# Optimization experiments

Hardware: AMD Instinct MI355X
Metric: run time of the kernel (lower is better)

The kernel has to match this reference:

```python
import jax, jax.numpy as jnp
import numpy as np

B, N, H = 128, 65536, 30  # batch, candidates per sample, horizon-7 steps


def setup_inputs() -> dict:
    key = jax.random.key(0)
    ks = jax.random.split(key, 8)
    proposal_feat = jax.random.normal(ks[0], (B, 64), dtype=jnp.float32)
    target_candidate = jax.random.normal(ks[1], (B, N, 2), dtype=jnp.float32)
    candidate = jax.random.normal(ks[2], (B * N, 2), dtype=jnp.float32)
    # confidence (class-1 prob) in [0.5, 1.0) so the mask conf[0] >= 0.5 keeps ALL n columns
    conf = 0.5 + 0.5 * jax.random.uniform(ks[3], (B, N), dtype=jnp.float32)
    RCNN_cls_result = jnp.stack([1.0 - conf, conf], axis=-1)  # [B, N, 2]
    offset = 0.1 * jax.random.normal(ks[4], (B, N, 2), dtype=jnp.float32)
    yaw_pred = jax.random.normal(ks[5], (B, 1), dtype=jnp.float32)
    y = jax.random.normal(ks[6], (B * H * 2,), dtype=jnp.float32)      # flat dx,dy deltas
    y_yaw = jax.random.normal(ks[7], (B * H,), dtype=jnp.float32)
    horizon = jnp.full((B,), H + 7, dtype=jnp.int32)  # all equal -> static shapes
    return {
        'proposal_feat': proposal_feat,
        'target_candidate': target_candidate,
        'candidate': candidate,
        'RCNN_cls_result': RCNN_cls_result,
        'offset': offset,
        'yaw_pred': yaw_pred,
        'y': y,
        'y_yaw': y_yaw,
        'horizon': horizon,
    }


def reference(proposal_feat, target_candidate, candidate, RCNN_cls_result,
              offset, yaw_pred, y, y_yaw, horizon):
    batch, n, _ = target_candidate.shape
    candidate_pos = candidate.reshape(batch, n, 2)
    # confidence filter: inputs guarantee conf[0] >= 0.5 everywhere -> keep all n
    conf = RCNN_cls_result[..., 1]                       # [B, n]
    order = jnp.argsort(-conf, axis=1)                   # descending per sample
    pred_pt = jnp.take_along_axis(candidate_pos, order[:, :, None], axis=1)  # [B, n, 2]
    pred_off = jnp.take_along_axis(offset, order[:, :, None], axis=1)        # [B, n, 2]
    pred_final = pred_pt + pred_off                      # [B, n, 2]
    # ground-truth endpoint: last element of per-sample cumsum of deltas == sum
    h = y.shape[0] // (batch * 2)                        # horizon - 7 (constant)
    gt_last = y.reshape(batch, h, 2).sum(axis=1)         # [B, 2]
    # loss_weight_by_dist branch: sum of squared distances gt_last vs every pred point
    d2 = jnp.sum((gt_last[:, None, :] - pred_final) ** 2, axis=-1)  # [B, n]
    loss = jnp.sum(d2).reshape(1)
    # clone is unmodified in the dist-weighted branch
    return RCNN_cls_result, loss
```

## Files before the change

kernel.cpp:

```cpp
#include <hip/hip_runtime.h>
#include <hip/hip_bf16.h>


typedef float v4f __attribute__((ext_vector_type(4)));

__global__ __launch_bounds__(256) void copy_and_loss_kernel(
    const v4f* __restrict__ cand,
    const v4f* __restrict__ off,
    const v4f* __restrict__ rcnn,
    v4f* __restrict__ out,
    const float* __restrict__ y,
    float* __restrict__ partials,
    int n4, int log_row4, int h)
{
    constexpr int U = 4;
    const size_t base = (size_t)blockIdx.x * (256 * U);
    const int b = (int)(base >> log_row4);

    float gx = 0.f, gy = 0.f;
    {
        const float2* yb = (const float2*)y + (size_t)b * h;
        for (int i = 0; i < h; ++i) { float2 v = yb[i]; gx += v.x; gy += v.y; }
    }

    float acc = 0.f;
    if (base + 256 * U <= (size_t)n4) {
        v4f c[U], o[U], r[U];
        #pragma unroll
        for (int u = 0; u < U; ++u) c[u] = cand[base + u * 256 + threadIdx.x];
        #pragma unroll
        for (int u = 0; u < U; ++u) o[u] = off[base + u * 256 + threadIdx.x];
        #pragma unroll
        for (int u = 0; u < U; ++u) r[u] = rcnn[base + u * 256 + threadIdx.x];
        #pragma unroll
        for (int u = 0; u < U; ++u) {
            __builtin_nontemporal_store(r[u], &out[base + u * 256 + threadIdx.x]);
            float dx0 = gx - (c[u].x + o[u].x);
            float dy0 = gy - (c[u].y + o[u].y);
            float dx1 = gx - (c[u].z + o[u].z);
            float dy1 = gy - (c[u].w + o[u].w);
            acc += dx0*dx0 + dy0*dy0 + dx1*dx1 + dy1*dy1;
        }
    } else {
        #pragma unroll
        for (int u = 0; u < U; ++u) {
            size_t idx = base + u * 256 + threadIdx.x;
            if (idx < (size_t)n4) {
                v4f c = cand[idx], o = off[idx], r = rcnn[idx];
                __builtin_nontemporal_store(r, &out[idx]);
                float dx0 = gx - (c.x + o.x);
                float dy0 = gy - (c.y + o.y);
                float dx1 = gx - (c.z + o.z);
                float dy1 = gy - (c.w + o.w);
                acc += dx0*dx0 + dy0*dy0 + dx1*dx1 + dy1*dy1;
            }
        }
    }

    #pragma unroll
    for (int s = 32; s > 0; s >>= 1) acc += __shfl_down(acc, s, 64);
    __shared__ float lds[4];
    int lane = threadIdx.x & 63, wid = threadIdx.x >> 6;
    if (lane == 0) lds[wid] = acc;
    __syncthreads();
    if (threadIdx.x == 0)
        partials[blockIdx.x] = lds[0] + lds[1] + lds[2] + lds[3];
}

__global__ __launch_bounds__(256) void final_reduce_kernel(
    const float* __restrict__ partials, float* __restrict__ loss_slot, int n)
{
    float acc = 0.f;
    for (int i = threadIdx.x; i < n; i += 256) acc += partials[i];
    #pragma unroll
    for (int s = 32; s > 0; s >>= 1) acc += __shfl_down(acc, s, 64);
    __shared__ float lds[4];
    int lane = threadIdx.x & 63, wid = threadIdx.x >> 6;
    if (lane == 0) lds[wid] = acc;
    __syncthreads();
    if (threadIdx.x == 0)
        *loss_slot = lds[0] + lds[1] + lds[2] + lds[3];
}

extern "C" void kernel_launch(void* const* d_in, const int* in_sizes, int n_in,
                              void* d_out, int out_size, void* d_ws, size_t ws_size,
                              hipStream_t stream) {
    const float* candidate = (const float*)d_in[2];
    const float* rcnn      = (const float*)d_in[3];
    const float* offset    = (const float*)d_in[4];
    const float* y         = (const float*)d_in[6];

    const int B = in_sizes[8];
    const int N = in_sizes[3] / (B * 2);
    const int h = in_sizes[6] / (B * 2);

    float* out_f     = (float*)d_out;
    float* loss_slot = out_f + (size_t)B * N * 2;
    float* partials  = (float*)d_ws;

    const int n4 = (B * N * 2) / 4;
    const int row4 = N / 2;
    int log_row4 = 0;
    while ((1 << log_row4) < row4) ++log_row4;

    const int block = 256;
    constexpr int U = 4;
    const int grid = (n4 + block * U - 1) / (block * U);
    copy_and_loss_kernel<<<grid, block, 0, stream>>>(
        (const v4f*)candidate, (const v4f*)offset, (const v4f*)rcnn,
        (v4f*)d_out, y, partials, n4, log_row4, h);

    final_reduce_kernel<<<1, 256, 0, stream>>>(partials, loss_slot, grid);
}
```

Baseline: 263.5 us.

## Expand squared distance into moments and split copy from loss kernel

Rewrites the loss as sum(p^2) - 2*g·sum(p) + n*|g|^2 so the main kernel no longer needs per-sample ground truth. It drops the redundant per-block loop over y and moves the ground-truth sums into the single-block final kernel. The rcnn copy moves into its own grid-stride kernel, and loss blocks now each handle larger chunks. The trade-offs are an extra launch, reading inputs in two passes instead of one fused pass, and the cancellation risk of the expanded form in fp32.

```diff
diff --git a/kernel.cpp b/kernel.cpp
--- a/kernel.cpp
+++ b/kernel.cpp
@@ -1,85 +1,92 @@
 #include <hip/hip_runtime.h>
-#include <hip/hip_bf16.h>
 
 
 typedef float v4f __attribute__((ext_vector_type(4)));
 
-__global__ __launch_bounds__(256) void copy_and_loss_kernel(
-    const v4f* __restrict__ cand,
-    const v4f* __restrict__ off,
-    const v4f* __restrict__ rcnn,
-    v4f* __restrict__ out,
-    const float* __restrict__ y,
+__global__ __launch_bounds__(256) void rcnn_copy_kernel(
+    const v4f* __restrict__ rcnn, v4f* __restrict__ out, int n4)
+{
+    const int stride = gridDim.x * 256;
+    for (int i = blockIdx.x * 256 + threadIdx.x; i < n4; i += stride)
+        __builtin_nontemporal_store(rcnn[i], &out[i]);
+}
+
+__global__ __launch_bounds__(256) void loss_partials_kernel(
+    const v4f* __restrict__ cand, const v4f* __restrict__ off,
     float* __restrict__ partials,
-    int n4, int log_row4, int h)
+    int chunk, int nblk)
 {
-    constexpr int U = 4;
-    const size_t base = (size_t)blockIdx.x * (256 * U);
-    const int b = (int)(base >> log_row4);
+    const int base = blockIdx.x * chunk;
+    float s2 = 0.f, s1x = 0.f, s1y = 0.f;
+    for (int i = base + threadIdx.x; i < base + chunk; i += 256) {
+        v4f c = cand[i], o = off[i];
+        float px0 = c.x + o.x, py0 = c.y + o.y;
+        float px1 = c.z + o.z, py1 = c.w + o.w;
+        s2  += px0 * px0; s2 += py0 * py0;
+        s2  += px1 * px1; s2 += py1 * py1;
+        s1x += px0 + px1;
+        s1y += py0 + py1;
+    }
+    #pragma unroll
+    for (int s = 32; s > 0; s >>= 1) {
+        s2  += __shfl_down(s2,  s, 64);
+        s1x += __shfl_down(s1x, s, 64);
+        s1y += __shfl_down(s1y, s, 64);
+    }
+    __shared__ float lds[12];
+    int lane = threadIdx.x & 63, wid = threadIdx.x >> 6;
+    if (lane == 0) { lds[wid] = s2; lds[4 + wid] = s1x; lds[8 + wid] = s1y; }
+    __syncthreads();
+    if (threadIdx.x == 0) {
+        partials[blockIdx.x]            = lds[0] + lds[1] + lds[2]  + lds[3];
+        partials[nblk + blockIdx.x]     = lds[4] + lds[5] + lds[6]  + lds[7];
+        partials[2 * nblk + blockIdx.x] = lds[8] + lds[9] + lds[10] + lds[11];
+    }
+}
 
-    float gx = 0.f, gy = 0.f;
-    {
-        const float2* yb = (const float2*)y + (size_t)b * h;
-        for (int i = 0; i < h; ++i) { float2 v = yb[i]; gx += v.x; gy += v.y; }
+__global__ __launch_bounds__(256) void final_reduce_gt_kernel(
+    const float* __restrict__ partials, const float* __restrict__ y,
+    float* __restrict__ loss_slot,
+    int nblk, int B, int h, int row4, int chunk)
+{
+    extern __shared__ float dyn[];
+    float* yld = dyn;
+    float* gt  = dyn + B * h * 2;
+
+    const int ytot = B * h * 2;
+    for (int i = threadIdx.x; i < ytot; i += 256) yld[i] = y[i];
+    __syncthreads();
+
+    for (int b = threadIdx.x; b < B; b += 256) {
+        float gx = 0.f, gy = 0.f;
+        const float* yr = yld + (size_t)b * h * 2;
+        for (int i = 0; i < h; ++i) { gx += yr[2 * i]; gy += yr[2 * i + 1]; }
+        gt[2 * b] = gx; gt[2 * b + 1] = gy;
     }
+    __syncthreads();
 
+    const int blocks_per_b = row4 / chunk;
+    const float cnt_b = (float)(row4 * 2);
     float acc = 0.f;
-    if (base + 256 * U <= (size_t)n4) {
-        v4f c[U], o[U], r[U];
-        #pragma unroll
-        for (int u = 0; u < U; ++u) c[u] = cand[base + u * 256 + threadIdx.x];
-        #pragma unroll
-        for (int u = 0; u < U; ++u) o[u] = off[base + u * 256 + threadIdx.x];
-        #pragma unroll
-        for (int u = 0; u < U; ++u) r[u] = rcnn[base + u * 256 + threadIdx.x];
-        #pragma unroll
-        for (int u = 0; u < U; ++u) {
-            __builtin_nontemporal_store(r[u], &out[base + u * 256 + threadIdx.x]);
-            float dx0 = gx - (c[u].x + o[u].x);
-            float dy0 = gy - (c[u].y + o[u].y);
-            float dx1 = gx - (c[u].z + o[u].z);
-            float dy1 = gy - (c[u].w + o[u].w);
-            acc += dx0*dx0 + dy0*dy0 + dx1*dx1 + dy1*dy1;
-        }
-    } else {
-        #pragma unroll
-        for (int u = 0; u < U; ++u) {
-            size_t idx = base + u * 256 + threadIdx.x;
-            if (idx < (size_t)n4) {
-                v4f c = cand[idx], o = off[idx], r = rcnn[idx];
-                __builtin_nontemporal_store(r, &out[idx]);
-                float dx0 = gx - (c.x + o.x);
-                float dy0 = gy - (c.y + o.y);
-                float dx1 = gx - (c.z + o.z);
-                float dy1 = gy - (c.w + o.w);
-                acc += dx0*dx0 + dy0*dy0 + dx1*dx1 + dy1*dy1;
-            }
-        }
+    for (int k = threadIdx.x; k < nblk; k += 256) {
+        int b = k / blocks_per_b;
+        float gx = gt[2 * b], gy = gt[2 * b + 1];
+        acc += partials[k]
+             - 2.f * (gx * partials[nblk + k] + gy * partials[2 * nblk + k]);
+    }
+    for (int b = threadIdx.x; b < B; b += 256) {
+        float gx = gt[2 * b], gy = gt[2 * b + 1];
+        acc += cnt_b * (gx * gx + gy * gy);
     }
 
     #pragma unroll
     for (int s = 32; s > 0; s >>= 1) acc += __shfl_down(acc, s, 64);
-    __shared__ float lds[4];
+    __shared__ float red[4];
     int lane = threadIdx.x & 63, wid = threadIdx.x >> 6;
-    if (lane == 0) lds[wid] = acc;
+    if (lane == 0) red[wid] = acc;
     __syncthreads();
     if (threadIdx.x == 0)
-        partials[blockIdx.x] = lds[0] + lds[1] + lds[2] + lds[3];
-}
-
-__global__ __launch_bounds__(256) void final_reduce_kernel(
-    const float* __restrict__ partials, float* __restrict__ loss_slot, int n)
-{
-    float acc = 0.f;
-    for (int i = threadIdx.x; i < n; i += 256) acc += partials[i];
-    #pragma unroll
-    for (int s = 32; s > 0; s >>= 1) acc += __shfl_down(acc, s, 64);
-    __shared__ float lds[4];
-    int lane = threadIdx.x & 63, wid = threadIdx.x >> 6;
-    if (lane == 0) lds[wid] = acc;
-    __syncthreads();
-    if (threadIdx.x == 0)
-        *loss_slot = lds[0] + lds[1] + lds[2] + lds[3];
+        *loss_slot = red[0] + red[1] + red[2] + red[3];
 }
 
 extern "C" void kernel_launch(void* const* d_in, const int* in_sizes, int n_in,
@@ -98,17 +105,19 @@
     float* loss_slot = out_f + (size_t)B * N * 2;
     float* partials  = (float*)d_ws;
 
-    const int n4 = (B * N * 2) / 4;
+    const int n4   = (B * N * 2) / 4;
     const int row4 = N / 2;
-    int log_row4 = 0;
-    while ((1 << log_row4) < row4) ++log_row4;
+    int chunk = 2048;
+    while (row4 % chunk) chunk >>= 1;
+    const int nblk = n4 / chunk;
 
-    const int block = 256;
-    constexpr int U = 4;
-    const int grid = (n4 + block * U - 1) / (block * U);
-    copy_and_loss_kernel<<<grid, block, 0, stream>>>(
-        (const v4f*)candidate, (const v4f*)offset, (const v4f*)rcnn,
-        (v4f*)d_out, y, partials, n4, log_row4, h);
+    loss_partials_kernel<<<nblk, 256, 0, stream>>>(
+        (const v4f*)candidate, (const v4f*)offset, partials, chunk, nblk);
 
-    final_reduce_kernel<<<1, 256, 0, stream>>>(partials, loss_slot, grid);
+    rcnn_copy_kernel<<<2048, 256, 0, stream>>>(
+        (const v4f*)rcnn, (v4f*)d_out, n4);
+
+    const size_t shmem = (size_t)(B * h * 2 + 2 * B) * sizeof(float);
+    final_reduce_gt_kernel<<<1, 256, shmem, stream>>>(
+        partials, y, loss_slot, nblk, B, h, row4, chunk);
 }
```

Measured after the change: 267.9 us. No clear change (+1.7%).
